# Optimization experiments

Measured on AMD Instinct MI355X. Metric: run time of the kernel, lower is better.

Reference implementation:

```python
import jax, jax.numpy as jnp
import numpy as np

B, T, N, F = 64, 512, 14, 16
H_LSTM, H_GCN = 128, 64


def setup_inputs() -> dict:
    key = jax.random.key(0)
    ks = jax.random.split(key, 12)
    s = 0.05
    return {
        "x": jax.random.normal(ks[0], (B, T, N, F), dtype=jnp.float32),
        "adj": jax.random.uniform(ks[1], (N, N), dtype=jnp.float32),
        "W_ih": jax.random.normal(ks[2], (4 * H_LSTM, F), dtype=jnp.float32) * s,
        "W_hh": jax.random.normal(ks[3], (4 * H_LSTM, H_LSTM), dtype=jnp.float32) * s,
        "b_ih": jax.random.normal(ks[4], (4 * H_LSTM,), dtype=jnp.float32) * s,
        "b_hh": jax.random.normal(ks[5], (4 * H_LSTM,), dtype=jnp.float32) * s,
        "W_gcn": jax.random.normal(ks[6], (H_GCN, H_LSTM), dtype=jnp.float32) * s,
        "b_gcn": jax.random.normal(ks[7], (H_GCN,), dtype=jnp.float32) * s,
        "W_out": jax.random.normal(ks[8], (1, H_GCN), dtype=jnp.float32) * s,
        "b_out": jax.random.normal(ks[9], (1,), dtype=jnp.float32) * s,
        "W_lin1": jax.random.normal(ks[10], (28, N), dtype=jnp.float32) * s,
        "b_lin1": jax.random.normal(ks[11], (28,), dtype=jnp.float32) * s,
    }


def _lstm_last(x_seq, W_ih, W_hh, b_ih, b_hh):
    # x_seq: [M, T, F]; single-layer LSTM, torch gate order (i, f, g, o).
    M = x_seq.shape[0]
    H = W_hh.shape[1]
    # Precompute input contribution for all timesteps: [T, M, 4H]
    xw = jnp.einsum('mtf,gf->tmg', x_seq, W_ih) + b_ih + b_hh

    def step(carry, xt):
        h, c = carry
        gates = xt + h @ W_hh.T
        i, f, g, o = jnp.split(gates, 4, axis=-1)
        i = jax.nn.sigmoid(i)
        f = jax.nn.sigmoid(f)
        g = jnp.tanh(g)
        o = jax.nn.sigmoid(o)
        c = f * c + i * g
        h = o * jnp.tanh(c)
        return (h, c), None

    h0 = jnp.zeros((M, H), dtype=x_seq.dtype)
    (h_last, _), _ = jax.lax.scan(step, (h0, h0), xw)
    return h_last  # [M, H]


def reference(x, adj, W_ih, W_hh, b_ih, b_hh, W_gcn, b_gcn, W_out, b_out, W_lin1, b_lin1):
    Bb, Tt, Nn, Ff = x.shape
    # Batch all N node sequences into one recurrent pass (same math as per-node loop).
    x_nodes = x.transpose(0, 2, 1, 3).reshape(Bb * Nn, Tt, Ff)  # [B*N, T, F]
    h_last = _lstm_last(x_nodes, W_ih, W_hh, b_ih, b_hh)        # [B*N, H]
    lstm_out = h_last.reshape(Bb, Nn, -1)                        # [B, N, H]

    # Normalized adjacency with self-loops: D^-1/2 (A+I) D^-1/2
    A_hat = adj + jnp.eye(Nn, dtype=adj.dtype)
    d = A_hat.sum(axis=1) ** -0.5
    A_norm = d[:, None] * A_hat * d[None, :]

    x_gcn = jnp.einsum('ij,bjk->bik', A_norm, lstm_out)          # [B, N, H]
    x_gcn = jax.nn.relu(x_gcn @ W_gcn.T + b_gcn)                 # [B, N, H_GCN]
    x_gcn = (x_gcn @ W_out.T + b_out).squeeze(-1)                # [B, N]
    out = jax.nn.sigmoid(x_gcn @ W_lin1.T + b_lin1)              # [B, 28]
    return out
```

## Files before the change

### kernel.cpp

```cpp
#include <hip/hip_runtime.h>
#include <hip/hip_bf16.h>

#define B_   64
#define T_   512
#define N_   14
#define F_   16
#define H_   128
#define G4_  512
#define TCH  64
#define MBLK 4
#define NBLK 224

typedef __attribute__((ext_vector_type(8))) short bfrag;
typedef __attribute__((ext_vector_type(4))) float facc;
typedef __attribute__((ext_vector_type(4))) int   v4i;

#define L2E   1.4426950408889634f
#define L2E2  2.8853900817779268f

#define SX   0
#define SH   16384
#define LDSZ 17408

__device__ __forceinline__ short f2bf(float f) {
    unsigned u = __builtin_bit_cast(unsigned, f);
    return (short)((u + 0x7FFFu + ((u >> 16) & 1u)) >> 16);
}
__device__ __forceinline__ float bf2f(unsigned short s) {
    return __builtin_bit_cast(float, (unsigned)s << 16);
}
__device__ __forceinline__ unsigned cvt_pk_bf16(float a, float b) {
    unsigned r;
    asm("v_cvt_pk_bf16_f32 %0, %1, %2" : "=v"(r) : "v"(a), "v"(b));
    return r;
}
__device__ __forceinline__ float ex2n(float x) {
    float r;
    asm("v_exp_f32_e64 %0, -%1" : "=v"(r) : "v"(x));
    return r;
}
__device__ __forceinline__ v4i mfma_i8(v4i a, v4i b, v4i c) {
    v4i d;
    asm("v_mfma_i32_16x16x64_i8 %0, %1, %2, %3"
        : "=&v"(d) : "v"(a), "v"(b), "v"(c));
    return d;
}
__device__ __forceinline__ void bar() {
    asm volatile("s_waitcnt lgkmcnt(0)" ::: "memory");
    __builtin_amdgcn_s_barrier();
    asm volatile("" ::: "memory");
}

__global__ void prep1_kernel(const float* __restrict__ W_hh,
                             const float* __restrict__ b_ih, const float* __restrict__ b_hh,
                             float* __restrict__ inv127, float* __restrict__ sw,
                             float* __restrict__ bias) {
    const int g = threadIdx.x;
    float mx = 0.0f;
    for (int k = 0; k < H_; ++k) mx = fmaxf(mx, fabsf(W_hh[g * H_ + k]));
    const float sc = (g >= 256 && g < 384) ? L2E2 : L2E;
    inv127[g] = 127.0f / mx;
    sw[g]     = mx * sc * (1.0f / 16129.0f);
    bias[g]   = (b_ih[g] + b_hh[g]) * sc;
}

__global__ void prep2_kernel(const float* __restrict__ W_hh, const float* __restrict__ W_ih,
                             const float* __restrict__ inv127,
                             signed char* __restrict__ w8, short* __restrict__ wih_bf) {
    const int i = blockIdx.x * blockDim.x + threadIdx.x;
    if (i < G4_ * H_)
        w8[i] = (signed char)(int)rintf(W_hh[i] * inv127[i >> 7]);
    if (i < G4_ * 32) {
        const int n = i >> 5, k = i & 31;
        const float sc = (n >= 256 && n < 384) ? L2E2 : L2E;
        wih_bf[i] = (k < F_) ? f2bf(W_ih[n * F_ + k] * sc) : (short)0;
    }
}

template<int P, bool PREF>
__device__ __forceinline__ void lstm_step(char* lds, int tl,
    const v4i (&B8)[4][2], const bfrag (&Bx)[4], const facc (&bsp)[4],
    const float (&sw4)[4], facc (&xacc)[2][4], float& cc,
    int hrd, int xrd, int wboff)
{
    bar();
    const char* hb = lds + SH + P * 512;
    const v4i a0 = *(const v4i*)(hb + hrd);
    const v4i a1 = *(const v4i*)(hb + hrd + 256);
    bfrag ax;
    if (PREF) ax = *(const bfrag*)(lds + SX + (tl + 1) * 256 + xrd);

    const v4i z4 = (v4i){0, 0, 0, 0};
    v4i p[4], r[4];
    __builtin_amdgcn_s_setprio(1);
#pragma unroll
    for (int q = 0; q < 4; ++q) p[q] = mfma_i8(a0, B8[q][0], z4);
#pragma unroll
    for (int q = 0; q < 4; ++q) r[q] = mfma_i8(a1, B8[q][1], z4);
    __builtin_amdgcn_s_setprio(0);

    float z[4];
#pragma unroll
    for (int q = 0; q < 4; ++q)
        z[q] = (float)(p[q][0] + r[q][0]) * sw4[q] + xacc[P][q][0];

    const float ea = ex2n(z[0]);
    const float ef = ex2n(z[1]);
    const float eo = ex2n(z[3]);
    const float eg = ex2n(fabsf(z[2]));
    const float d1 = (1.0f + ea) * (1.0f + eg);
    const float d2 = 1.0f + ef;
    const float rP = __builtin_amdgcn_rcpf(d1 * d2);
    const float ig = __builtin_copysignf((1.0f - eg) * (rP * d2), z[2]);
    cc = (rP * d1) * cc + ig;
    const float ec = ex2n(L2E2 * fabsf(cc));
    const float hv = __builtin_copysignf(
        (1.0f - ec) * __builtin_amdgcn_rcpf((1.0f + eo) * (1.0f + ec)), cc);
    *(signed char*)(lds + SH + (P ^ 1) * 512 + wboff) =
        (signed char)(int)rintf(hv * 127.0f);

    if (PREF) {
#pragma unroll
        for (int q = 0; q < 4; ++q)
            xacc[P ^ 1][q] = __builtin_amdgcn_mfma_f32_16x16x32_bf16(ax, Bx[q], bsp[q], 0, 0, 0);
    }
}

__global__ __launch_bounds__(512, 2) void lstm_kernel(
    const float* __restrict__ x,
    const signed char* __restrict__ w8,
    const short* __restrict__ wih_bf,
    const float* __restrict__ bias,
    const float* __restrict__ sw,
    unsigned short* __restrict__ h_out)
{
    const int m0  = blockIdx.x * MBLK;
    const int tid = threadIdx.x;
    const int w   = tid >> 6, l = tid & 63;
    const int lr  = l & 15, lk = l >> 4;
    const int hcol = w * 16 + lr;

    __shared__ __align__(16) char lds[LDSZ];

    v4i   B8[4][2];
    bfrag Bx[4];
    facc  bsp[4];
    float sw4[4];
#pragma unroll
    for (int q = 0; q < 4; ++q) {
        const int n = q * H_ + hcol;
#pragma unroll
        for (int ks = 0; ks < 2; ++ks)
            B8[q][ks] = *(const v4i*)(w8 + n * 128 + ks * 64 + lk * 16);
        Bx[q] = *(const bfrag*)(wih_bf + n * 32 + lk * 8);
        const float b = bias[n];
        bsp[q] = (facc){b, b, b, b};
        sw4[q] = sw[n];
    }
#pragma unroll
    for (int q = 0; q < 4; ++q) {
        asm volatile("" : "+v"(B8[q][0]));
        asm volatile("" : "+v"(B8[q][1]));
        asm volatile("" : "+v"(Bx[q]));
        asm volatile("" : "+v"(bsp[q]));
    }

    const int hrd = lk * 64 + (lr >> 2) * 16;
    const int xrd = (lr >> 2) * 64 + lk * 16;
    const int wboff = w * 64 + lk * 16 + lr;

    const int skb = tid & 1, sseq = (tid >> 1) & 3, stl = tid >> 3;
    const int seqg = m0 + sseq;
    const int bb = seqg / N_, nn = seqg % N_;
    const float* xq = x + (((size_t)bb * T_ + stl) * N_ + nn) * F_ + skb * 8;
    const int sbyte = SX + stl * 256 + sseq * 64 + skb * 16;

    for (int i = tid; i < LDSZ / 4; i += 512) ((int*)lds)[i] = 0;
    float4 p0 = *(const float4*)xq, p1 = *(const float4*)(xq + 4);

    float cc = 0.0f;
    facc  xacc[2][4];
    bar();

#pragma unroll 1
    for (int chunk = 0; chunk < T_ / TCH; ++chunk) {
        {
            uint4 o;
            o.x = cvt_pk_bf16(p0.x, p0.y); o.y = cvt_pk_bf16(p0.z, p0.w);
            o.z = cvt_pk_bf16(p1.x, p1.y); o.w = cvt_pk_bf16(p1.z, p1.w);
            *(uint4*)(lds + sbyte) = o;
        }
        if (chunk + 1 < T_ / TCH) {
            xq += TCH * N_ * F_;
            p0 = *(const float4*)xq; p1 = *(const float4*)(xq + 4);
        }
        bar();

        {
            const bfrag ax = *(const bfrag*)(lds + SX + xrd);
#pragma unroll
            for (int q = 0; q < 4; ++q)
                xacc[0][q] = __builtin_amdgcn_mfma_f32_16x16x32_bf16(ax, Bx[q], bsp[q], 0, 0, 0);
        }

#pragma unroll 1
        for (int tl = 0; tl < TCH; tl += 2) {
            lstm_step<0, true>(lds, tl, B8, Bx, bsp, sw4, xacc, cc,
                               hrd, xrd, wboff);
            if (tl + 2 < TCH)
                lstm_step<1, true>(lds, tl + 1, B8, Bx, bsp, sw4, xacc, cc,
                                   hrd, xrd, wboff);
            else
                lstm_step<1, false>(lds, tl + 1, B8, Bx, bsp, sw4, xacc, cc,
                                    hrd, xrd, wboff);
        }
    }
    bar();

    {
        const int g = tid >> 7, c = tid & 127;
        const int addr = SH + (c >> 4) * 64 + g * 16 + (c & 15);
        const signed char v = *(const signed char*)(lds + addr);
        h_out[(size_t)(m0 + g) * H_ + c] = f2bf((float)v * (1.0f / 127.0f));
    }
}

__global__ __launch_bounds__(256) void head_kernel(
    const float* __restrict__ adj,
    const float* __restrict__ W_gcn, const float* __restrict__ b_gcn,
    const float* __restrict__ W_out, const float* __restrict__ b_out,
    const float* __restrict__ W_lin1, const float* __restrict__ b_lin1,
    const unsigned short* __restrict__ h_in,
    float* __restrict__ out)
{
    const int b   = blockIdx.x;
    const int tid = threadIdx.x;

    __shared__ float s_A[N_][N_];
    __shared__ float s_d[N_];
    __shared__ float s_h[N_][H_];
    __shared__ float s_xg[N_][H_];
    __shared__ float s_g1[N_][64];
    __shared__ float s_s[N_];

    for (int idx = tid; idx < N_ * H_; idx += 256)
        s_h[idx >> 7][idx & 127] = bf2f(h_in[(size_t)b * N_ * H_ + idx]);

    if (tid < N_) {
        float sum = 0.0f;
        for (int j = 0; j < N_; ++j)
            sum += adj[tid * N_ + j] + (tid == j ? 1.0f : 0.0f);
        s_d[tid] = rsqrtf(sum);
    }
    __syncthreads();

    if (tid < N_ * N_) {
        const int i = tid / N_, j = tid % N_;
        const float a = adj[i * N_ + j] + (i == j ? 1.0f : 0.0f);
        s_A[i][j] = s_d[i] * a * s_d[j];
    }
    __syncthreads();

    for (int idx = tid; idx < N_ * H_; idx += 256) {
        const int i = idx >> 7, k = idx & 127;
        float acc = 0.0f;
#pragma unroll
        for (int j = 0; j < N_; ++j) acc += s_A[i][j] * s_h[j][k];
        s_xg[i][k] = acc;
    }
    __syncthreads();

    for (int idx = tid; idx < N_ * 64; idx += 256) {
        const int i = idx >> 6, q = idx & 63;
        float a0 = 0.f, a1 = 0.f, a2 = 0.f, a3 = 0.f;
#pragma unroll
        for (int k = 0; k < H_; k += 4) {
            a0 += s_xg[i][k+0] * W_gcn[q * H_ + k+0];
            a1 += s_xg[i][k+1] * W_gcn[q * H_ + k+1];
            a2 += s_xg[i][k+2] * W_gcn[q * H_ + k+2];
            a3 += s_xg[i][k+3] * W_gcn[q * H_ + k+3];
        }
        const float acc = b_gcn[q] + ((a0 + a1) + (a2 + a3));
        s_g1[i][q] = fmaxf(acc, 0.0f);
    }
    __syncthreads();

    if (tid < N_) {
        float acc = b_out[0];
#pragma unroll
        for (int q = 0; q < 64; ++q) acc += s_g1[tid][q] * W_out[q];
        s_s[tid] = acc;
    }
    __syncthreads();

    if (tid < 28) {
        float acc = b_lin1[tid];
#pragma unroll
        for (int i = 0; i < N_; ++i) acc += s_s[i] * W_lin1[tid * N_ + i];
        out[b * 28 + tid] = 1.0f / (1.0f + __expf(-acc));
    }
}

extern "C" void kernel_launch(void* const* d_in, const int* in_sizes, int n_in,
                              void* d_out, int out_size, void* d_ws, size_t ws_size,
                              hipStream_t stream) {
    const float* x      = (const float*)d_in[0];
    const float* adj    = (const float*)d_in[1];
    const float* W_ih   = (const float*)d_in[2];
    const float* W_hh   = (const float*)d_in[3];
    const float* b_ih   = (const float*)d_in[4];
    const float* b_hh   = (const float*)d_in[5];
    const float* W_gcn  = (const float*)d_in[6];
    const float* b_gcn  = (const float*)d_in[7];
    const float* W_out  = (const float*)d_in[8];
    const float* b_out  = (const float*)d_in[9];
    const float* W_lin1 = (const float*)d_in[10];
    const float* b_lin1 = (const float*)d_in[11];
    float* out = (float*)d_out;

    char* ws = (char*)d_ws;
    signed char*    w8     = (signed char*)(ws);
    short*          wih_bf = (short*)(ws + 65536);
    float*          bias   = (float*)(ws + 98304);
    float*          sw     = (float*)(ws + 100352);
    float*          inv127 = (float*)(ws + 102400);
    unsigned short* h_last = (unsigned short*)(ws + 104448);

    prep1_kernel<<<1, 512, 0, stream>>>(W_hh, b_ih, b_hh, inv127, sw, bias);
    prep2_kernel<<<128, 512, 0, stream>>>(W_hh, W_ih, inv127, w8, wih_bf);
    lstm_kernel<<<NBLK, 512, 0, stream>>>(x, w8, wih_bf, bias, sw, h_last);
    head_kernel<<<B_, 256, 0, stream>>>(adj, W_gcn, b_gcn, W_out, b_out,
                                        W_lin1, b_lin1, h_last, out);
}
```

Measured before the change: 213.0 us.

## Interleave two independent sequence groups per block to hide recurrent step latency

Each block now processes 8 sequences as two groups of 4 and halves the grid. Each half-step issues the int8 recurrent MFMAs for one group while running the other group's gate nonlinearities and h store, a software pipeline across independent recurrences. The goal is to fill the latency of the serial MFMA-to-epilogue dependency within a single block. In exchange, LDS use doubles, launch bounds drop to one block per CU, there are twice as many barriers per timestep, and only 112 blocks run. A magic-number float trick replaces rintf for the int8 quantization of h.

```diff
diff --git a/kernel.cpp b/kernel.cpp
--- a/kernel.cpp
+++ b/kernel.cpp
@@ -8,8 +8,8 @@
 #define H_   128
 #define G4_  512
 #define TCH  64
-#define MBLK 4
-#define NBLK 224
+#define MBLK 8
+#define NBLK 112
 
 typedef __attribute__((ext_vector_type(8))) short bfrag;
 typedef __attribute__((ext_vector_type(4))) float facc;
@@ -18,9 +18,11 @@
 #define L2E   1.4426950408889634f
 #define L2E2  2.8853900817779268f
 
-#define SX   0
-#define SH   16384
-#define LDSZ 17408
+#define SXA  0
+#define SXB  16384
+#define SHA  32768
+#define SHB  33280
+#define LDSZ 33792
 
 __device__ __forceinline__ short f2bf(float f) {
     unsigned u = __builtin_bit_cast(unsigned, f);
@@ -49,6 +51,10 @@
     asm volatile("s_waitcnt lgkmcnt(0)" ::: "memory");
     __builtin_amdgcn_s_barrier();
     asm volatile("" ::: "memory");
+}
+__device__ __forceinline__ signed char rint8(float hv) {
+    const float m = __builtin_fmaf(hv, 127.0f, 12582912.0f);
+    return (signed char)__builtin_bit_cast(unsigned, m);
 }
 
 __global__ void prep1_kernel(const float* __restrict__ W_hh,
@@ -77,33 +83,14 @@
     }
 }
 
-template<int P, bool PREF>
-__device__ __forceinline__ void lstm_step(char* lds, int tl,
-    const v4i (&B8)[4][2], const bfrag (&Bx)[4], const facc (&bsp)[4],
-    const float (&sw4)[4], facc (&xacc)[2][4], float& cc,
-    int hrd, int xrd, int wboff)
+__device__ __forceinline__ void epilogue(char* lds, int shO, int wboff,
+    const int (&accS)[4], const float (&xaccS)[4], const float (&sw4)[4],
+    float& cc)
 {
-    bar();
-    const char* hb = lds + SH + P * 512;
-    const v4i a0 = *(const v4i*)(hb + hrd);
-    const v4i a1 = *(const v4i*)(hb + hrd + 256);
-    bfrag ax;
-    if (PREF) ax = *(const bfrag*)(lds + SX + (tl + 1) * 256 + xrd);
-
-    const v4i z4 = (v4i){0, 0, 0, 0};
-    v4i p[4], r[4];
-    __builtin_amdgcn_s_setprio(1);
-#pragma unroll
-    for (int q = 0; q < 4; ++q) p[q] = mfma_i8(a0, B8[q][0], z4);
-#pragma unroll
-    for (int q = 0; q < 4; ++q) r[q] = mfma_i8(a1, B8[q][1], z4);
-    __builtin_amdgcn_s_setprio(0);
-
     float z[4];
 #pragma unroll
     for (int q = 0; q < 4; ++q)
-        z[q] = (float)(p[q][0] + r[q][0]) * sw4[q] + xacc[P][q][0];
-
+        z[q] = (float)accS[q] * sw4[q] + xaccS[q];
     const float ea = ex2n(z[0]);
     const float ef = ex2n(z[1]);
     const float eo = ex2n(z[3]);
@@ -116,17 +103,44 @@
     const float ec = ex2n(L2E2 * fabsf(cc));
     const float hv = __builtin_copysignf(
         (1.0f - ec) * __builtin_amdgcn_rcpf((1.0f + eo) * (1.0f + ec)), cc);
-    *(signed char*)(lds + SH + (P ^ 1) * 512 + wboff) =
-        (signed char)(int)rintf(hv * 127.0f);
-
-    if (PREF) {
-#pragma unroll
-        for (int q = 0; q < 4; ++q)
-            xacc[P ^ 1][q] = __builtin_amdgcn_mfma_f32_16x16x32_bf16(ax, Bx[q], bsp[q], 0, 0, 0);
-    }
-}
-
-__global__ __launch_bounds__(512, 2) void lstm_kernel(
+    *(signed char*)(lds + shO + wboff) = rint8(hv);
+}
+
+__device__ __forceinline__ void half_step(char* lds, int tl,
+    int shM, int shO, int sxM,
+    const v4i (&B8)[4][2], const bfrag (&Bx)[4], const facc (&bsp)[4],
+    const float (&sw4)[4],
+    int (&accS_M)[4], float (&xaccS_M)[4],
+    const int (&accS_O)[4], const float (&xaccS_O)[4], float& ccO,
+    int hrd, int xrd, int wboff)
+{
+    bar();
+    const v4i a0 = *(const v4i*)(lds + shM + hrd);
+    const v4i a1 = *(const v4i*)(lds + shM + hrd + 256);
+    const bfrag ax = *(const bfrag*)(lds + sxM + tl * 256 + xrd);
+
+    const v4i z4 = (v4i){0, 0, 0, 0};
+    v4i p[4], r[4];
+    __builtin_amdgcn_s_setprio(1);
+#pragma unroll
+    for (int q = 0; q < 4; ++q) p[q] = mfma_i8(a0, B8[q][0], z4);
+#pragma unroll
+    for (int q = 0; q < 4; ++q) r[q] = mfma_i8(a1, B8[q][1], z4);
+    __builtin_amdgcn_s_setprio(0);
+
+    epilogue(lds, shO, wboff, accS_O, xaccS_O, sw4, ccO);
+
+    facc xt[4];
+#pragma unroll
+    for (int q = 0; q < 4; ++q)
+        xt[q] = __builtin_amdgcn_mfma_f32_16x16x32_bf16(ax, Bx[q], bsp[q], 0, 0, 0);
+#pragma unroll
+    for (int q = 0; q < 4; ++q) accS_M[q] = p[q][0] + r[q][0];
+#pragma unroll
+    for (int q = 0; q < 4; ++q) xaccS_M[q] = xt[q][0];
+}
+
+__global__ __launch_bounds__(512, 1) void lstm_kernel(
     const float* __restrict__ x,
     const signed char* __restrict__ w8,
     const short* __restrict__ wih_bf,
@@ -170,58 +184,67 @@
     const int wboff = w * 64 + lk * 16 + lr;
 
     const int skb = tid & 1, sseq = (tid >> 1) & 3, stl = tid >> 3;
-    const int seqg = m0 + sseq;
-    const int bb = seqg / N_, nn = seqg % N_;
-    const float* xq = x + (((size_t)bb * T_ + stl) * N_ + nn) * F_ + skb * 8;
-    const int sbyte = SX + stl * 256 + sseq * 64 + skb * 16;
+    const int seqA = m0 + sseq, seqB = m0 + 4 + sseq;
+    const int bbA = seqA / N_, nnA = seqA % N_;
+    const int bbB = seqB / N_, nnB = seqB % N_;
+    const float* xqA = x + (((size_t)bbA * T_ + stl) * N_ + nnA) * F_ + skb * 8;
+    const float* xqB = x + (((size_t)bbB * T_ + stl) * N_ + nnB) * F_ + skb * 8;
+    const int sbyteA = SXA + stl * 256 + sseq * 64 + skb * 16;
+    const int sbyteB = SXB + stl * 256 + sseq * 64 + skb * 16;
 
     for (int i = tid; i < LDSZ / 4; i += 512) ((int*)lds)[i] = 0;
-    float4 p0 = *(const float4*)xq, p1 = *(const float4*)(xq + 4);
-
-    float cc = 0.0f;
-    facc  xacc[2][4];
-    bar();
+    float4 pA0 = *(const float4*)xqA, pA1 = *(const float4*)(xqA + 4);
+    float4 pB0 = *(const float4*)xqB, pB1 = *(const float4*)(xqB + 4);
+
+    float ccA = 0.0f, ccB = 0.0f;
+    int   accS_A[4], accS_B[4];
+    float xaccS_A[4], xaccS_B[4];
+#pragma unroll
+    for (int q = 0; q < 4; ++q) {
+        accS_B[q] = 0; xaccS_B[q] = 0.0f;
+        accS_A[q] = 0; xaccS_A[q] = 0.0f;
+    }
 
 #pragma unroll 1
     for (int chunk = 0; chunk < T_ / TCH; ++chunk) {
+        bar();
         {
-            uint4 o;
-            o.x = cvt_pk_bf16(p0.x, p0.y); o.y = cvt_pk_bf16(p0.z, p0.w);
-            o.z = cvt_pk_bf16(p1.x, p1.y); o.w = cvt_pk_bf16(p1.z, p1.w);
-            *(uint4*)(lds + sbyte) = o;
+            uint4 oa, ob;
+            oa.x = cvt_pk_bf16(pA0.x, pA0.y); oa.y = cvt_pk_bf16(pA0.z, pA0.w);
+            oa.z = cvt_pk_bf16(pA1.x, pA1.y); oa.w = cvt_pk_bf16(pA1.z, pA1.w);
+            ob.x = cvt_pk_bf16(pB0.x, pB0.y); ob.y = cvt_pk_bf16(pB0.z, pB0.w);
+            ob.z = cvt_pk_bf16(pB1.x, pB1.y); ob.w = cvt_pk_bf16(pB1.z, pB1.w);
+            *(uint4*)(lds + sbyteA) = oa;
+            *(uint4*)(lds + sbyteB) = ob;
         }
         if (chunk + 1 < T_ / TCH) {
-            xq += TCH * N_ * F_;
-            p0 = *(const float4*)xq; p1 = *(const float4*)(xq + 4);
+            xqA += TCH * N_ * F_; xqB += TCH * N_ * F_;
+            pA0 = *(const float4*)xqA; pA1 = *(const float4*)(xqA + 4);
+            pB0 = *(const float4*)xqB; pB1 = *(const float4*)(xqB + 4);
         }
-        bar();
-
-        {
-            const bfrag ax = *(const bfrag*)(lds + SX + xrd);
-#pragma unroll
-            for (int q = 0; q < 4; ++q)
-                xacc[0][q] = __builtin_amdgcn_mfma_f32_16x16x32_bf16(ax, Bx[q], bsp[q], 0, 0, 0);
+
+#pragma unroll 1
+        for (int tl = 0; tl < TCH; ++tl) {
+            half_step(lds, tl, SHA, SHB, SXA, B8, Bx, bsp, sw4,
+                      accS_A, xaccS_A, accS_B, xaccS_B, ccB,
+                      hrd, xrd, wboff);
+            half_step(lds, tl, SHB, SHA, SXB, B8, Bx, bsp, sw4,
+                      accS_B, xaccS_B, accS_A, xaccS_A, ccA,
+                      hrd, xrd, wboff);
         }
-
-#pragma unroll 1
-        for (int tl = 0; tl < TCH; tl += 2) {
-            lstm_step<0, true>(lds, tl, B8, Bx, bsp, sw4, xacc, cc,
-                               hrd, xrd, wboff);
-            if (tl + 2 < TCH)
-                lstm_step<1, true>(lds, tl + 1, B8, Bx, bsp, sw4, xacc, cc,
-                                   hrd, xrd, wboff);
-            else
-                lstm_step<1, false>(lds, tl + 1, B8, Bx, bsp, sw4, xacc, cc,
-                                    hrd, xrd, wboff);
-        }
-    }
+    }
+
     bar();
-
-    {
-        const int g = tid >> 7, c = tid & 127;
-        const int addr = SH + (c >> 4) * 64 + g * 16 + (c & 15);
+    epilogue(lds, SHB, wboff, accS_B, xaccS_B, sw4, ccB);
+    bar();
+
+#pragma unroll
+    for (int e0 = 0; e0 < 2; ++e0) {
+        const int e = tid + e0 * 512;
+        const int G = e >> 9, s = (e >> 7) & 3, c = e & 127;
+        const int addr = (G ? SHB : SHA) + (c >> 4) * 64 + s * 16 + (c & 15);
         const signed char v = *(const signed char*)(lds + addr);
-        h_out[(size_t)(m0 + g) * H_ + c] = f2bf((float)v * (1.0f / 127.0f));
+        h_out[(size_t)(m0 + G * 4 + s) * H_ + c] = f2bf((float)v * (1.0f / 127.0f));
     }
 }
 
```

Result: slower. 391.9 us (+84.0%).
